# Optimization experiments

Hardware: AMD Instinct MI355X
Metric: run time of the kernel (lower is better)

The kernel has to match this reference:

```python
import jax, jax.numpy as jnp
import numpy as np

B, S, D = 4, 2048, 512
QKD = 256
HID = 3 * D  # expansion_factor=3
EPS = 1e-5


def _ln(x, g, b):
    m = jnp.mean(x, axis=-1, keepdims=True)
    v = jnp.mean((x - m) ** 2, axis=-1, keepdims=True)
    return (x - m) * jax.lax.rsqrt(v + EPS) * g + b


def setup_inputs() -> dict:
    key = jax.random.key(0)
    ks = jax.random.split(key, 12)
    s = lambda fan: 1.0 / np.sqrt(fan)
    return {
        "x":  jax.random.normal(ks[0], (B, S, D), jnp.float32),
        "Wm": jax.random.uniform(ks[1], (D, D), jnp.float32, -s(D), s(D)),
        "bm": jnp.zeros((D,), jnp.float32),
        "g1": jnp.ones((D,), jnp.float32),
        "b1": jnp.zeros((D,), jnp.float32),
        "Wh": jax.random.uniform(ks[2], (2 * HID, D), jnp.float32, -s(D), s(D)),
        "bh": jnp.zeros((2 * HID,), jnp.float32),
        "Wq": jax.random.uniform(ks[3], (QKD, D), jnp.float32, -s(D), s(D)),
        "bq": jnp.zeros((QKD,), jnp.float32),
        "Wb": jax.random.normal(ks[4], (QKD, QKD), jnp.float32),
        "Wo": jax.random.uniform(ks[5], (D, HID), jnp.float32, -s(HID), s(HID)),
        "bo": jnp.zeros((D,), jnp.float32),
        "g2": jnp.ones((D,), jnp.float32),
        "b2": jnp.zeros((D,), jnp.float32),
    }


def reference(x, Wm, bm, g1, b1, Wh, bh, Wq, bq, Wb, Wo, bo, g2, b2):
    seq_len = x.shape[-2]
    memory = jnp.einsum('bsd,ed->bse', x, Wm) + bm
    normed = _ln(x + memory, g1, b1)
    h = jax.nn.relu(jnp.einsum('bsd,hd->bsh', normed, Wh) + bh)
    v, gate = h[..., :HID], h[..., HID:]
    Z = jax.nn.relu(jnp.einsum('bsd,qd->bsq', normed, Wq) + bq)  # [B,S,QKD]
    QK = jnp.einsum('bid,de,bje->bij', Z, Wb, Z) / seq_len
    A = jax.nn.relu(QK) ** 2  # relu^2 attention, no softmax
    V = jnp.einsum('bij,bjd->bid', A, v) * gate
    out = _ln(jnp.einsum('bsh,dh->bsd', V, Wo) + bo, g2, b2)
    return out + x
```

## Files before the change

kernel.cpp:

```cpp
#include <hip/hip_runtime.h>

typedef unsigned short u16;
typedef unsigned char u8;
typedef __attribute__((ext_vector_type(8))) short short8;
typedef __attribute__((ext_vector_type(4))) float f32x4;
typedef __attribute__((ext_vector_type(8))) int int8v;
typedef __attribute__((ext_vector_type(4))) int int4v;

#define LN_EPS 1e-5f
#define SCALE_A 4096.f
#define SCALE_V 8.f
#define INV_SCALE_AV (1.f/32768.f)
#define MX_ONE 0x7F7F7F7Fu

__device__ __forceinline__ u16 f2bf(float f){
    union { float f; unsigned u; } c; c.f = f;
    unsigned u = c.u + 0x7FFFu + ((c.u >> 16) & 1u);
    return (u16)(u >> 16);
}
__device__ __forceinline__ float bf2f(u16 h){
    union { unsigned u; float f; } c; c.u = ((unsigned)h) << 16;
    return c.f;
}
__device__ __forceinline__ u8 f2fp8(float f){
    int r = __builtin_amdgcn_cvt_pk_fp8_f32(f, 0.f, 0, false);
    return (u8)(r & 0xFF);
}

enum { EPI_NONE=0, EPI_BIAS_RES, EPI_RELUSQ };
enum { OT_F32=0, OT_BF16=1, OT_FP8=2 };

__device__ __forceinline__ void gl2lds16(const void* g, void* lds){
    __builtin_amdgcn_global_load_lds(
        (const __attribute__((address_space(1))) unsigned*)g,
        (__attribute__((address_space(3))) unsigned*)lds, 16, 0, 0);
}

template<int EPI, int OT>
__global__ __launch_bounds__(256)
void mgemm(const u16* __restrict__ A, const u16* __restrict__ B, void* __restrict__ Cv,
           int K, int lda, int ldb, int ldc,
           long sAb, long sBb, long sCb,
           const float* __restrict__ bias,
           const float* __restrict__ ext, int ldext,
           float scale)
{
    __shared__ u16 sA[2][4096];
    __shared__ u16 sB[2][4096];
    const int tid = threadIdx.x;
    const int m0 = blockIdx.y * 128, n0 = blockIdx.x * 128;
    const int z  = blockIdx.z;
    const u16* Az = A + (size_t)z * sAb;
    const u16* Bz = B + (size_t)z * sBb;

    const int lane = tid & 63, quad = lane >> 4, l15 = lane & 15;
    const int wave = tid >> 6;
    const int wm = (wave >> 1) * 64, wn = (wave & 1) * 64;

    const u16* gA[2]; const u16* gB[2]; int lo[2];
#pragma unroll
    for (int r = 0; r < 2; r++){
        const int c = tid + r * 256;
        gA[r] = Az + (size_t)(m0 + (c & 127)) * lda + (c >> 7) * 8;
        gB[r] = Bz + (size_t)(n0 + (c & 127)) * ldb + (c >> 7) * 8;
        lo[r] = ((tid & 192) + r * 256) * 16;
    }

    auto stage = [&](int buf, int k0){
#pragma unroll
        for (int r = 0; r < 2; r++){
            gl2lds16(gA[r] + k0, (char*)sA[buf] + lo[r]);
            gl2lds16(gB[r] + k0, (char*)sB[buf] + lo[r]);
        }
    };

    f32x4 acc[4][4];
#pragma unroll
    for (int i = 0; i < 4; i++)
#pragma unroll
        for (int j = 0; j < 4; j++) acc[i][j] = (f32x4){0.f,0.f,0.f,0.f};

    stage(0, 0);
    int buf = 0;
    for (int k0 = 0; k0 < K; k0 += 32){
        __syncthreads();
        if (k0 + 32 < K) stage(buf ^ 1, k0 + 32);
        const u16* fA = sA[buf] + quad * 1024 + (wm + l15) * 8;
        const u16* fB = sB[buf] + quad * 1024 + (wn + l15) * 8;
        short8 a[4], b[4];
#pragma unroll
        for (int t = 0; t < 4; t++){
            a[t] = *(const short8*)(fA + t * 128);
            b[t] = *(const short8*)(fB + t * 128);
        }
#pragma unroll
        for (int i = 0; i < 4; i++)
#pragma unroll
            for (int j = 0; j < 4; j++)
                acc[i][j] = __builtin_amdgcn_mfma_f32_16x16x32_bf16(a[i], b[j], acc[i][j], 0, 0, 0);
        buf ^= 1;
    }

    float* Cf = (float*)Cv; u16* Ch = (u16*)Cv; u8* C8 = (u8*)Cv;
    const size_t zc = (size_t)z * sCb;
#pragma unroll
    for (int i = 0; i < 4; i++){
#pragma unroll
        for (int j = 0; j < 4; j++){
            const int n = n0 + wn + j * 16 + l15;
            float bs = (EPI==EPI_BIAS_RES) ? bias[n] : 0.f;
#pragma unroll
            for (int r = 0; r < 4; r++){
                const int m = m0 + wm + i * 16 + quad * 4 + r;
                float v = acc[i][j][r] + bs;
                if (EPI==EPI_BIAS_RES)
                    v += ext[(size_t)m * ldext + n];
                if (EPI==EPI_RELUSQ){ float t = fmaxf(v * scale, 0.f); v = t * t * SCALE_A; }
                if (OT==OT_FP8)       C8[zc + (size_t)m * ldc + n] = f2fp8(v);
                else if (OT==OT_BF16) Ch[zc + (size_t)m * ldc + n] = f2bf(v);
                else                  Cf[zc + (size_t)m * ldc + n] = v;
            }
        }
    }
}

__global__ __launch_bounds__(256)
void mgemm_dual(const u16* __restrict__ Anrm, const u16* __restrict__ Wh,
                const u16* __restrict__ Wq,
                const float* __restrict__ bh, const float* __restrict__ bq,
                u8* __restrict__ v8, u16* __restrict__ gbf, u16* __restrict__ Zb)
{
    __shared__ u16 sA[2][4096];
    __shared__ u16 sB[2][4096];
    const int tid = threadIdx.x;
    const bool isZ = blockIdx.x >= 24;
    const u16* Bm = isZ ? Wq : Wh;
    const float* bias = isZ ? bq : bh;
    const int m0 = blockIdx.y * 128;
    const int n0 = (isZ ? (blockIdx.x - 24) : blockIdx.x) * 128;
    const int K = 512, lda = 512, ldb = 512;

    const int lane = tid & 63, quad = lane >> 4, l15 = lane & 15;
    const int wave = tid >> 6;
    const int wm = (wave >> 1) * 64, wn = (wave & 1) * 64;

    const u16* gA[2]; const u16* gB[2]; int lo[2];
#pragma unroll
    for (int r = 0; r < 2; r++){
        const int c = tid + r * 256;
        gA[r] = Anrm + (size_t)(m0 + (c & 127)) * lda + (c >> 7) * 8;
        gB[r] = Bm   + (size_t)(n0 + (c & 127)) * ldb + (c >> 7) * 8;
        lo[r] = ((tid & 192) + r * 256) * 16;
    }
    auto stage = [&](int buf, int k0){
#pragma unroll
        for (int r = 0; r < 2; r++){
            gl2lds16(gA[r] + k0, (char*)sA[buf] + lo[r]);
            gl2lds16(gB[r] + k0, (char*)sB[buf] + lo[r]);
        }
    };

    f32x4 acc[4][4];
#pragma unroll
    for (int i = 0; i < 4; i++)
#pragma unroll
        for (int j = 0; j < 4; j++) acc[i][j] = (f32x4){0.f,0.f,0.f,0.f};

    stage(0, 0);
    int buf = 0;
    for (int k0 = 0; k0 < K; k0 += 32){
        __syncthreads();
        if (k0 + 32 < K) stage(buf ^ 1, k0 + 32);
        const u16* fA = sA[buf] + quad * 1024 + (wm + l15) * 8;
        const u16* fB = sB[buf] + quad * 1024 + (wn + l15) * 8;
        short8 a[4], b[4];
#pragma unroll
        for (int t = 0; t < 4; t++){
            a[t] = *(const short8*)(fA + t * 128);
            b[t] = *(const short8*)(fB + t * 128);
        }
#pragma unroll
        for (int i = 0; i < 4; i++)
#pragma unroll
            for (int j = 0; j < 4; j++)
                acc[i][j] = __builtin_amdgcn_mfma_f32_16x16x32_bf16(a[i], b[j], acc[i][j], 0, 0, 0);
        buf ^= 1;
    }

#pragma unroll
    for (int i = 0; i < 4; i++){
#pragma unroll
        for (int j = 0; j < 4; j++){
            const int n = n0 + wn + j * 16 + l15;
            const float bs = bias[n];
#pragma unroll
            for (int r = 0; r < 4; r++){
                const int m = m0 + wm + i * 16 + quad * 4 + r;
                float v = fmaxf(acc[i][j][r] + bs, 0.f);
                if (isZ)            Zb[(size_t)m * 256 + n] = f2bf(v);
                else if (n < 1536)  v8[(size_t)m * 1536 + n] = f2fp8(v * SCALE_V);
                else                gbf[(size_t)m * 1536 + n - 1536] = f2bf(v);
            }
        }
    }
}

__global__ __launch_bounds__(256)
void mgemm8mx(const u8* __restrict__ A, const u8* __restrict__ B, u16* __restrict__ C,
              int K, int lda, int ldb, int ldc,
              long sAb, long sBb, long sCb,
              const u16* __restrict__ gate, int ldext, long sEb)
{
    __shared__ u8 sA[16384];
    __shared__ u8 sB[16384];
    const int tid = threadIdx.x;
    const int m0 = blockIdx.y * 128, n0 = blockIdx.x * 128;
    const int z  = blockIdx.z;
    const u8* Az = A + (size_t)z * sAb;
    const u8* Bz = B + (size_t)z * sBb;

    const int lane = tid & 63, quad = lane >> 4, l15 = lane & 15;
    const int wave = tid >> 6;
    const int wm = (wave >> 1) * 64, wn = (wave & 1) * 64;

    const u8* gA[4]; const u8* gB[4]; int lo[4];
#pragma unroll
    for (int p = 0; p < 4; p++){
        const int r = p * 32 + (tid >> 3);
        const int j = (tid & 7) ^ (r & 7);
        gA[p] = Az + (size_t)(m0 + r) * lda + j * 16;
        gB[p] = Bz + (size_t)(n0 + r) * ldb + j * 16;
        lo[p] = p * 4096 + wave * 1024;
    }

    f32x4 acc[4][4];
#pragma unroll
    for (int i = 0; i < 4; i++)
#pragma unroll
        for (int j = 0; j < 4; j++) acc[i][j] = (f32x4){0.f,0.f,0.f,0.f};

    for (int k0 = 0; k0 < K; k0 += 128){
#pragma unroll
        for (int p = 0; p < 4; p++){
            gl2lds16(gA[p] + k0, (char*)sA + lo[p]);
            gl2lds16(gB[p] + k0, (char*)sB + lo[p]);
        }
        __syncthreads();
        int8v a[4], b[4];
#pragma unroll
        for (int i = 0; i < 4; i++){
            const int m = wm + i * 16 + l15;
            const int4v a0 = *(const int4v*)(sA + m * 128 + ((2*quad    ) ^ (m & 7)) * 16);
            const int4v a1 = *(const int4v*)(sA + m * 128 + ((2*quad + 1) ^ (m & 7)) * 16);
            a[i] = (int8v){a0[0],a0[1],a0[2],a0[3],a1[0],a1[1],a1[2],a1[3]};
            const int n = wn + i * 16 + l15;
            const int4v b0 = *(const int4v*)(sB + n * 128 + ((2*quad    ) ^ (n & 7)) * 16);
            const int4v b1 = *(const int4v*)(sB + n * 128 + ((2*quad + 1) ^ (n & 7)) * 16);
            b[i] = (int8v){b0[0],b0[1],b0[2],b0[3],b1[0],b1[1],b1[2],b1[3]};
        }
#pragma unroll
        for (int i = 0; i < 4; i++)
#pragma unroll
            for (int j = 0; j < 4; j++)
                acc[i][j] = __builtin_amdgcn_mfma_scale_f32_16x16x128_f8f6f4(
                    a[i], b[j], acc[i][j], 0, 0, 0, MX_ONE, 0, MX_ONE);
        __syncthreads();
    }

    const size_t zc = (size_t)z * sCb;
#pragma unroll
    for (int i = 0; i < 4; i++){
#pragma unroll
        for (int j = 0; j < 4; j++){
            const int n = n0 + wn + j * 16 + l15;
#pragma unroll
            for (int r = 0; r < 4; r++){
                const int m = m0 + wm + i * 16 + quad * 4 + r;
                float v = acc[i][j][r] * INV_SCALE_AV
                        * bf2f(gate[(size_t)z * sEb + (size_t)m * ldext + n]);
                C[zc + (size_t)m * ldc + n] = f2bf(v);
            }
        }
    }
}

template<bool OUT_BF, bool POST_RES, int NSUM, bool PRE_RES>
__global__ __launch_bounds__(256)
void ln_k(const float* __restrict__ in, const float* __restrict__ g,
          const float* __restrict__ b, const float* __restrict__ res_post,
          const float* __restrict__ res_pre, const float* __restrict__ bias2,
          long pstride, void* __restrict__ out)
{
    const int row = blockIdx.x, tid = threadIdx.x;
    const size_t base = (size_t)row * 512 + tid * 2;
    float2 v = *(const float2*)(in + base);
#pragma unroll
    for (int p = 1; p < NSUM; p++){
        const float2 w = *(const float2*)(in + (size_t)p * pstride + base);
        v.x += w.x; v.y += w.y;
    }
    if (NSUM > 1){
        const float2 bb2 = *(const float2*)(bias2 + tid * 2);
        v.x += bb2.x; v.y += bb2.y;
    }
    if (PRE_RES){
        const float2 r = *(const float2*)(res_pre + base);
        v.x += r.x; v.y += r.y;
    }
    float s = v.x + v.y, ss = v.x * v.x + v.y * v.y;
#pragma unroll
    for (int off = 32; off > 0; off >>= 1){
        s  += __shfl_down(s,  off);
        ss += __shfl_down(ss, off);
    }
    __shared__ float sbuf[8], ssbuf[8];
    const int wid = tid >> 6, lane = tid & 63;
    if (lane == 0){ sbuf[wid] = s; ssbuf[wid] = ss; }
    __syncthreads();
    if (tid == 0){
        float S = 0.f, SS = 0.f;
#pragma unroll
        for (int i = 0; i < 4; i++){ S += sbuf[i]; SS += ssbuf[i]; }
        const float mean = S * (1.f/512.f);
        const float var  = SS * (1.f/512.f) - mean * mean;
        sbuf[4]  = mean;
        ssbuf[4] = rsqrtf(var + LN_EPS);
    }
    __syncthreads();
    const float mean = sbuf[4], rstd = ssbuf[4];
    const float2 gg = *(const float2*)(g + tid * 2);
    const float2 bb = *(const float2*)(b + tid * 2);
    float ox = (v.x - mean) * rstd * gg.x + bb.x;
    float oy = (v.y - mean) * rstd * gg.y + bb.y;
    if (POST_RES){
        const float2 r = *(const float2*)(res_post + base);
        ox += r.x; oy += r.y;
    }
    if (OUT_BF){
        unsigned pk = ((unsigned)f2bf(oy) << 16) | (unsigned)f2bf(ox);
        ((unsigned*)out)[(size_t)row * 256 + tid] = pk;
    } else {
        *(float2*)((float*)out + base) = make_float2(ox, oy);
    }
}

__global__ __launch_bounds__(256)
void castall_k(const float* __restrict__ x, const float* __restrict__ Wm,
               const float* __restrict__ Wh, const float* __restrict__ Wq,
               const float* __restrict__ Wo, const float* __restrict__ Wb,
               u16* __restrict__ xb, u16* __restrict__ Wmb, u16* __restrict__ Whb,
               u16* __restrict__ Wqb, u16* __restrict__ Wob, u16* __restrict__ WbT)
{
    const int i = blockIdx.x * 256 + threadIdx.x;
    if (i >= 1736704){
        const int j = i - 1736704;
        if (j < 65536){
            const int e = j >> 8, d = j & 255;
            WbT[e * 256 + d] = f2bf(Wb[d * 256 + e]);
        }
        return;
    }
    const float* src; u16* dst; int off;
    if      (i < 1048576){ src = x;  dst = xb;  off = i; }
    else if (i < 1114112){ src = Wm; dst = Wmb; off = i - 1048576; }
    else if (i < 1507328){ src = Wh; dst = Whb; off = i - 1114112; }
    else if (i < 1540096){ src = Wq; dst = Wqb; off = i - 1507328; }
    else                 { src = Wo; dst = Wob; off = i - 1540096; }
    const float4 v = ((const float4*)src)[off];
    ushort4 o; o.x = f2bf(v.x); o.y = f2bf(v.y); o.z = f2bf(v.z); o.w = f2bf(v.w);
    ((ushort4*)dst)[off] = o;
}

__global__ __launch_bounds__(256)
void tr8_k(const u8* __restrict__ v, u8* __restrict__ vT, int S, int HID){
    const int b = blockIdx.z;
    const int h0 = blockIdx.x * 64, s0 = blockIdx.y * 64;
    __shared__ u8 t[64][68];
    const u8* vb = v + (size_t)b * S * HID;
    u8* vTb = vT + (size_t)b * HID * S;
    const int tid = threadIdx.x;
#pragma unroll
    for (int i = 0; i < 4; i++){
        int idx = tid + i * 256;
        int r = idx >> 4, c4 = (idx & 15) * 4;
        uchar4 u = *(const uchar4*)(vb + (size_t)(s0 + r) * HID + h0 + c4);
        t[r][c4] = u.x; t[r][c4+1] = u.y; t[r][c4+2] = u.z; t[r][c4+3] = u.w;
    }
    __syncthreads();
#pragma unroll
    for (int i = 0; i < 4; i++){
        int idx = tid + i * 256;
        int r = idx >> 4, c4 = (idx & 15) * 4;
        uchar4 u;
        u.x = t[c4][r]; u.y = t[c4+1][r]; u.z = t[c4+2][r]; u.w = t[c4+3][r];
        *(uchar4*)(vTb + (size_t)(h0 + r) * S + s0 + c4) = u;
    }
}

extern "C" void kernel_launch(void* const* d_in, const int* in_sizes, int n_in,
                              void* d_out, int out_size, void* d_ws, size_t ws_size,
                              hipStream_t stream)
{
    const float* x  = (const float*)d_in[0];
    const float* Wm = (const float*)d_in[1];
    const float* bm = (const float*)d_in[2];
    const float* g1 = (const float*)d_in[3];
    const float* b1 = (const float*)d_in[4];
    const float* Wh = (const float*)d_in[5];
    const float* bh = (const float*)d_in[6];
    const float* Wq = (const float*)d_in[7];
    const float* bq = (const float*)d_in[8];
    const float* Wb = (const float*)d_in[9];
    const float* Wo = (const float*)d_in[10];
    const float* bo = (const float*)d_in[11];
    const float* g2 = (const float*)d_in[12];
    const float* b2 = (const float*)d_in[13];
    float* out = (float*)d_out;
    (void)in_sizes; (void)n_in; (void)out_size; (void)ws_size;

    const int Bn=4, S=2048, D=512, QKD=256, HID=1536, H2=3072;
    const int M = Bn * S;
    const long MD = (long)M * D;

    char* p = (char*)d_ws;
    auto alloc = [&](size_t bytes)->void*{ void* r = p; p += (bytes + 255) & ~(size_t)255; return r; };
    u16*  xbf  = (u16*) alloc((size_t)M*D*2);
    u16*  Wmbf = (u16*) alloc((size_t)D*D*2);
    u16*  Whbf = (u16*) alloc((size_t)H2*D*2);
    u16*  Wqbf = (u16*) alloc((size_t)QKD*D*2);
    u16*  Wobf = (u16*) alloc((size_t)D*HID*2);
    u16*  WbT  = (u16*) alloc((size_t)QKD*QKD*2);
    float* ybuf= (float*)alloc((size_t)MD*4*3);
    u16*  Zb   = (u16*) alloc((size_t)M*QKD*2);
    u16*  ZWbb = (u16*) alloc((size_t)M*QKD*2);
    u8*   v8   = (u8*)  alloc((size_t)M*HID);
    u16*  gbf  = (u16*) alloc((size_t)M*HID*2);
    u8*   vT8  = (u8*)  alloc((size_t)M*HID);
    u8*   A8   = (u8*)  alloc((size_t)M*S);
    u16*  Vgbf = (u16*) alloc((size_t)M*HID*2);
    u16*  nrm  = xbf;

    dim3 blk(256);

    castall_k<<<dim3(7040), blk, 0, stream>>>(x, Wm, Wh, Wq, Wo, Wb,
                                              xbf, Wmbf, Whbf, Wqbf, Wobf, WbT);
    mgemm<EPI_BIAS_RES,OT_F32><<<dim3(D/128, M/128, 1), blk, 0, stream>>>(
        xbf, Wmbf, ybuf, D, D, D, D, 0,0,0, bm, x, D, 1.f);
    ln_k<true,false,1,false><<<dim3(M), blk, 0, stream>>>(
        ybuf, g1, b1, nullptr, nullptr, nullptr, 0, nrm);
    mgemm_dual<<<dim3(26, M/128), blk, 0, stream>>>(
        nrm, Whbf, Wqbf, bh, bq, v8, gbf, Zb);
    mgemm<EPI_NONE,OT_BF16><<<dim3(QKD/128, M/128, 1), blk, 0, stream>>>(
        Zb, WbT, ZWbb, QKD, QKD, QKD, QKD, 0,0,0, nullptr, nullptr, 0, 1.f);
    mgemm<EPI_RELUSQ,OT_FP8><<<dim3(S/128, S/128, Bn), blk, 0, stream>>>(
        ZWbb, Zb, A8, QKD, QKD, QKD, S,
        (long)S*QKD, (long)S*QKD, (long)S*S,
        nullptr, nullptr, 0, 1.f/(float)S);
    tr8_k<<<dim3(HID/64, S/64, Bn), blk, 0, stream>>>(v8, vT8, S, HID);
    mgemm8mx<<<dim3(HID/128, S/128, Bn), blk, 0, stream>>>(
        A8, vT8, Vgbf, S, S, S, HID,
        (long)S*S, (long)HID*S, (long)S*HID,
        gbf, HID, (long)S*HID);
    mgemm<EPI_NONE,OT_F32><<<dim3(D/128, M/128, 3), blk, 0, stream>>>(
        Vgbf, Wobf, ybuf, HID/3, HID, HID, D, 512, 512, MD,
        nullptr, nullptr, 0, 1.f);
    ln_k<false,true,3,false><<<dim3(M), blk, 0, stream>>>(
        ybuf, g2, b2, x, nullptr, bo, MD, out);
}
```

Baseline: 341.7 us.

## Compute value projection in MX fp8 and rework GEMM staging and output split-K

The value half of the Wh projection now runs through the fp8 MX GEMM, fed by a new fp8 copy of the normed activations and fp8 Wh weights. Only the gate half and Wq stay in the bf16 dual GEMM. The bf16 GEMMs drop LDS double buffering in favour of a single buffer with two barriers per k-step, which lowers LDS use and may raise occupancy but removes load/compute overlap. The Wo projection changes from 3-way to 2-way split-K with bf16 partials, and the final layernorm is specialised, cutting intermediate memory traffic at some precision cost.

```diff
diff --git a/kernel.cpp b/kernel.cpp
--- a/kernel.cpp
+++ b/kernel.cpp
@@ -11,6 +11,9 @@
 #define SCALE_A 4096.f
 #define SCALE_V 8.f
 #define INV_SCALE_AV (1.f/32768.f)
+#define SCALE_NRM 4.f
+#define SCALE_WH 512.f
+#define INV_SCALE_H (1.f/2048.f)
 #define MX_ONE 0x7F7F7F7Fu
 
 __device__ __forceinline__ u16 f2bf(float f){
@@ -26,8 +29,12 @@
     int r = __builtin_amdgcn_cvt_pk_fp8_f32(f, 0.f, 0, false);
     return (u8)(r & 0xFF);
 }
-
-enum { EPI_NONE=0, EPI_BIAS_RES, EPI_RELUSQ };
+__device__ __forceinline__ u16 f2fp8x2(float a, float b){
+    int r = __builtin_amdgcn_cvt_pk_fp8_f32(a, b, 0, false);
+    return (u16)(r & 0xFFFF);
+}
+
+enum { EPI_NONE=0, EPI_BIAS_RES, EPI_BIAS_RELU, EPI_RELUSQ };
 enum { OT_F32=0, OT_BF16=1, OT_FP8=2 };
 
 __device__ __forceinline__ void gl2lds16(const void* g, void* lds){
@@ -45,8 +52,8 @@
            const float* __restrict__ ext, int ldext,
            float scale)
 {
-    __shared__ u16 sA[2][4096];
-    __shared__ u16 sB[2][4096];
+    __shared__ u16 sA[4096];
+    __shared__ u16 sB[4096];
     const int tid = threadIdx.x;
     const int m0 = blockIdx.y * 128, n0 = blockIdx.x * 128;
     const int z  = blockIdx.z;
@@ -66,27 +73,22 @@
         lo[r] = ((tid & 192) + r * 256) * 16;
     }
 
-    auto stage = [&](int buf, int k0){
+    f32x4 acc[4][4];
+#pragma unroll
+    for (int i = 0; i < 4; i++)
+#pragma unroll
+        for (int j = 0; j < 4; j++) acc[i][j] = (f32x4){0.f,0.f,0.f,0.f};
+
+    const u16* fA = sA + quad * 1024 + (wm + l15) * 8;
+    const u16* fB = sB + quad * 1024 + (wn + l15) * 8;
+
+    for (int k0 = 0; k0 < K; k0 += 32){
 #pragma unroll
         for (int r = 0; r < 2; r++){
-            gl2lds16(gA[r] + k0, (char*)sA[buf] + lo[r]);
-            gl2lds16(gB[r] + k0, (char*)sB[buf] + lo[r]);
-        }
-    };
-
-    f32x4 acc[4][4];
-#pragma unroll
-    for (int i = 0; i < 4; i++)
-#pragma unroll
-        for (int j = 0; j < 4; j++) acc[i][j] = (f32x4){0.f,0.f,0.f,0.f};
-
-    stage(0, 0);
-    int buf = 0;
-    for (int k0 = 0; k0 < K; k0 += 32){
+            gl2lds16(gA[r] + k0, (char*)sA + lo[r]);
+            gl2lds16(gB[r] + k0, (char*)sB + lo[r]);
+        }
         __syncthreads();
-        if (k0 + 32 < K) stage(buf ^ 1, k0 + 32);
-        const u16* fA = sA[buf] + quad * 1024 + (wm + l15) * 8;
-        const u16* fB = sB[buf] + quad * 1024 + (wn + l15) * 8;
         short8 a[4], b[4];
 #pragma unroll
         for (int t = 0; t < 4; t++){
@@ -98,7 +100,7 @@
 #pragma unroll
             for (int j = 0; j < 4; j++)
                 acc[i][j] = __builtin_amdgcn_mfma_f32_16x16x32_bf16(a[i], b[j], acc[i][j], 0, 0, 0);
-        buf ^= 1;
+        __syncthreads();
     }
 
     float* Cf = (float*)Cv; u16* Ch = (u16*)Cv; u8* C8 = (u8*)Cv;
@@ -108,13 +110,15 @@
 #pragma unroll
         for (int j = 0; j < 4; j++){
             const int n = n0 + wn + j * 16 + l15;
-            float bs = (EPI==EPI_BIAS_RES) ? bias[n] : 0.f;
+            float bs = (EPI==EPI_BIAS_RES || EPI==EPI_BIAS_RELU) ? bias[n] : 0.f;
 #pragma unroll
             for (int r = 0; r < 4; r++){
                 const int m = m0 + wm + i * 16 + quad * 4 + r;
                 float v = acc[i][j][r] + bs;
                 if (EPI==EPI_BIAS_RES)
                     v += ext[(size_t)m * ldext + n];
+                if (EPI==EPI_BIAS_RELU)
+                    v = fmaxf(v, 0.f);
                 if (EPI==EPI_RELUSQ){ float t = fmaxf(v * scale, 0.f); v = t * t * SCALE_A; }
                 if (OT==OT_FP8)       C8[zc + (size_t)m * ldc + n] = f2fp8(v);
                 else if (OT==OT_BF16) Ch[zc + (size_t)m * ldc + n] = f2bf(v);
@@ -125,19 +129,19 @@
 }
 
 __global__ __launch_bounds__(256)
-void mgemm_dual(const u16* __restrict__ Anrm, const u16* __restrict__ Wh,
+void mgemm_dual(const u16* __restrict__ Anrm, const u16* __restrict__ Whg,
                 const u16* __restrict__ Wq,
-                const float* __restrict__ bh, const float* __restrict__ bq,
-                u8* __restrict__ v8, u16* __restrict__ gbf, u16* __restrict__ Zb)
-{
-    __shared__ u16 sA[2][4096];
-    __shared__ u16 sB[2][4096];
+                const float* __restrict__ bhg, const float* __restrict__ bq,
+                u16* __restrict__ gbf, u16* __restrict__ Zb)
+{
+    __shared__ u16 sA[4096];
+    __shared__ u16 sB[4096];
     const int tid = threadIdx.x;
-    const bool isZ = blockIdx.x >= 24;
-    const u16* Bm = isZ ? Wq : Wh;
-    const float* bias = isZ ? bq : bh;
+    const bool isZ = blockIdx.x >= 12;
+    const u16* Bm = isZ ? Wq : Whg;
+    const float* bias = isZ ? bq : bhg;
     const int m0 = blockIdx.y * 128;
-    const int n0 = (isZ ? (blockIdx.x - 24) : blockIdx.x) * 128;
+    const int n0 = (isZ ? (blockIdx.x - 12) : blockIdx.x) * 128;
     const int K = 512, lda = 512, ldb = 512;
 
     const int lane = tid & 63, quad = lane >> 4, l15 = lane & 15;
@@ -152,27 +156,23 @@
         gB[r] = Bm   + (size_t)(n0 + (c & 127)) * ldb + (c >> 7) * 8;
         lo[r] = ((tid & 192) + r * 256) * 16;
     }
-    auto stage = [&](int buf, int k0){
+
+    f32x4 acc[4][4];
+#pragma unroll
+    for (int i = 0; i < 4; i++)
+#pragma unroll
+        for (int j = 0; j < 4; j++) acc[i][j] = (f32x4){0.f,0.f,0.f,0.f};
+
+    const u16* fA = sA + quad * 1024 + (wm + l15) * 8;
+    const u16* fB = sB + quad * 1024 + (wn + l15) * 8;
+
+    for (int k0 = 0; k0 < K; k0 += 32){
 #pragma unroll
         for (int r = 0; r < 2; r++){
-            gl2lds16(gA[r] + k0, (char*)sA[buf] + lo[r]);
-            gl2lds16(gB[r] + k0, (char*)sB[buf] + lo[r]);
-        }
-    };
-
-    f32x4 acc[4][4];
-#pragma unroll
-    for (int i = 0; i < 4; i++)
-#pragma unroll
-        for (int j = 0; j < 4; j++) acc[i][j] = (f32x4){0.f,0.f,0.f,0.f};
-
-    stage(0, 0);
-    int buf = 0;
-    for (int k0 = 0; k0 < K; k0 += 32){
+            gl2lds16(gA[r] + k0, (char*)sA + lo[r]);
+            gl2lds16(gB[r] + k0, (char*)sB + lo[r]);
+        }
         __syncthreads();
-        if (k0 + 32 < K) stage(buf ^ 1, k0 + 32);
-        const u16* fA = sA[buf] + quad * 1024 + (wm + l15) * 8;
-        const u16* fB = sB[buf] + quad * 1024 + (wn + l15) * 8;
         short8 a[4], b[4];
 #pragma unroll
         for (int t = 0; t < 4; t++){
@@ -184,7 +184,7 @@
 #pragma unroll
             for (int j = 0; j < 4; j++)
                 acc[i][j] = __builtin_amdgcn_mfma_f32_16x16x32_bf16(a[i], b[j], acc[i][j], 0, 0, 0);
-        buf ^= 1;
+        __syncthreads();
     }
 
 #pragma unroll
@@ -197,19 +197,20 @@
             for (int r = 0; r < 4; r++){
                 const int m = m0 + wm + i * 16 + quad * 4 + r;
                 float v = fmaxf(acc[i][j][r] + bs, 0.f);
-                if (isZ)            Zb[(size_t)m * 256 + n] = f2bf(v);
-                else if (n < 1536)  v8[(size_t)m * 1536 + n] = f2fp8(v * SCALE_V);
-                else                gbf[(size_t)m * 1536 + n - 1536] = f2bf(v);
+                if (isZ) Zb[(size_t)m * 256 + n] = f2bf(v);
+                else     gbf[(size_t)m * 1536 + n] = f2bf(v);
             }
         }
     }
 }
 
+template<bool VOUT>
 __global__ __launch_bounds__(256)
 void mgemm8mx(const u8* __restrict__ A, const u8* __restrict__ B, u16* __restrict__ C,
               int K, int lda, int ldb, int ldc,
               long sAb, long sBb, long sCb,
-              const u16* __restrict__ gate, int ldext, long sEb)
+              const u16* __restrict__ gate, int ldext, long sEb,
+              const float* __restrict__ bias, u8* __restrict__ vout)
 {
     __shared__ u8 sA[16384];
     __shared__ u8 sB[16384];
@@ -276,37 +277,26 @@
 #pragma unroll
             for (int r = 0; r < 4; r++){
                 const int m = m0 + wm + i * 16 + quad * 4 + r;
-                float v = acc[i][j][r] * INV_SCALE_AV
-                        * bf2f(gate[(size_t)z * sEb + (size_t)m * ldext + n]);
-                C[zc + (size_t)m * ldc + n] = f2bf(v);
+                if (VOUT){
+                    float h = fmaxf(acc[i][j][r] * INV_SCALE_H + bias[n], 0.f);
+                    vout[(size_t)m * 1536 + n] = f2fp8(h * SCALE_V);
+                } else {
+                    float v = acc[i][j][r] * INV_SCALE_AV
+                            * bf2f(gate[(size_t)z * sEb + (size_t)m * ldext + n]);
+                    C[zc + (size_t)m * ldc + n] = f2bf(v);
+                }
             }
         }
     }
 }
 
-template<bool OUT_BF, bool POST_RES, int NSUM, bool PRE_RES>
-__global__ __launch_bounds__(256)
-void ln_k(const float* __restrict__ in, const float* __restrict__ g,
-          const float* __restrict__ b, const float* __restrict__ res_post,
-          const float* __restrict__ res_pre, const float* __restrict__ bias2,
-          long pstride, void* __restrict__ out)
+__global__ __launch_bounds__(256)
+void ln1_k(const float* __restrict__ in, const float* __restrict__ g,
+           const float* __restrict__ b, u16* __restrict__ nbf, u16* __restrict__ n8)
 {
     const int row = blockIdx.x, tid = threadIdx.x;
     const size_t base = (size_t)row * 512 + tid * 2;
-    float2 v = *(const float2*)(in + base);
-#pragma unroll
-    for (int p = 1; p < NSUM; p++){
-        const float2 w = *(const float2*)(in + (size_t)p * pstride + base);
-        v.x += w.x; v.y += w.y;
-    }
-    if (NSUM > 1){
-        const float2 bb2 = *(const float2*)(bias2 + tid * 2);
-        v.x += bb2.x; v.y += bb2.y;
-    }
-    if (PRE_RES){
-        const float2 r = *(const float2*)(res_pre + base);
-        v.x += r.x; v.y += r.y;
-    }
+    const float2 v = *(const float2*)(in + base);
     float s = v.x + v.y, ss = v.x * v.x + v.y * v.y;
 #pragma unroll
     for (int off = 32; off > 0; off >>= 1){
@@ -330,25 +320,63 @@
     const float mean = sbuf[4], rstd = ssbuf[4];
     const float2 gg = *(const float2*)(g + tid * 2);
     const float2 bb = *(const float2*)(b + tid * 2);
-    float ox = (v.x - mean) * rstd * gg.x + bb.x;
-    float oy = (v.y - mean) * rstd * gg.y + bb.y;
-    if (POST_RES){
-        const float2 r = *(const float2*)(res_post + base);
-        ox += r.x; oy += r.y;
-    }
-    if (OUT_BF){
-        unsigned pk = ((unsigned)f2bf(oy) << 16) | (unsigned)f2bf(ox);
-        ((unsigned*)out)[(size_t)row * 256 + tid] = pk;
-    } else {
-        *(float2*)((float*)out + base) = make_float2(ox, oy);
-    }
+    const float ox = (v.x - mean) * rstd * gg.x + bb.x;
+    const float oy = (v.y - mean) * rstd * gg.y + bb.y;
+    ((unsigned*)nbf)[(size_t)row * 256 + tid] =
+        ((unsigned)f2bf(oy) << 16) | (unsigned)f2bf(ox);
+    n8[(size_t)row * 256 + tid] = f2fp8x2(ox * SCALE_NRM, oy * SCALE_NRM);
+}
+
+__global__ __launch_bounds__(256)
+void ln2_k(const u16* __restrict__ pa, long pstride,
+           const float* __restrict__ bias2,
+           const float* __restrict__ g, const float* __restrict__ b,
+           const float* __restrict__ x, float* __restrict__ out)
+{
+    const int row = blockIdx.x, tid = threadIdx.x;
+    const size_t base = (size_t)row * 512 + tid * 2;
+    const unsigned p0 = ((const unsigned*)pa)[(size_t)row * 256 + tid];
+    const unsigned p1 = ((const unsigned*)(pa + pstride))[(size_t)row * 256 + tid];
+    const float2 bb2 = *(const float2*)(bias2 + tid * 2);
+    float2 v;
+    v.x = bf2f((u16)p0) + bf2f((u16)p1) + bb2.x;
+    v.y = bf2f((u16)(p0 >> 16)) + bf2f((u16)(p1 >> 16)) + bb2.y;
+    float s = v.x + v.y, ss = v.x * v.x + v.y * v.y;
+#pragma unroll
+    for (int off = 32; off > 0; off >>= 1){
+        s  += __shfl_down(s,  off);
+        ss += __shfl_down(ss, off);
+    }
+    __shared__ float sbuf[8], ssbuf[8];
+    const int wid = tid >> 6, lane = tid & 63;
+    if (lane == 0){ sbuf[wid] = s; ssbuf[wid] = ss; }
+    __syncthreads();
+    if (tid == 0){
+        float S = 0.f, SS = 0.f;
+#pragma unroll
+        for (int i = 0; i < 4; i++){ S += sbuf[i]; SS += ssbuf[i]; }
+        const float mean = S * (1.f/512.f);
+        const float var  = SS * (1.f/512.f) - mean * mean;
+        sbuf[4]  = mean;
+        ssbuf[4] = rsqrtf(var + LN_EPS);
+    }
+    __syncthreads();
+    const float mean = sbuf[4], rstd = ssbuf[4];
+    const float2 gg = *(const float2*)(g + tid * 2);
+    const float2 bb = *(const float2*)(b + tid * 2);
+    const float2 r = *(const float2*)(x + base);
+    float2 o;
+    o.x = (v.x - mean) * rstd * gg.x + bb.x + r.x;
+    o.y = (v.y - mean) * rstd * gg.y + bb.y + r.y;
+    *(float2*)(out + base) = o;
 }
 
 __global__ __launch_bounds__(256)
 void castall_k(const float* __restrict__ x, const float* __restrict__ Wm,
                const float* __restrict__ Wh, const float* __restrict__ Wq,
                const float* __restrict__ Wo, const float* __restrict__ Wb,
-               u16* __restrict__ xb, u16* __restrict__ Wmb, u16* __restrict__ Whb,
+               u16* __restrict__ xb, u16* __restrict__ Wmb, u8* __restrict__ Wh8,
+               u16* __restrict__ Whgb,
                u16* __restrict__ Wqb, u16* __restrict__ Wob, u16* __restrict__ WbT)
 {
     const int i = blockIdx.x * 256 + threadIdx.x;
@@ -360,12 +388,20 @@
         }
         return;
     }
+    if (i >= 1114112 && i < 1310720){
+        const int off = i - 1114112;
+        const float4 v = ((const float4*)Wh)[off];
+        unsigned r0 = (unsigned)f2fp8x2(v.x * SCALE_WH, v.y * SCALE_WH);
+        unsigned r1 = (unsigned)f2fp8x2(v.z * SCALE_WH, v.w * SCALE_WH);
+        ((unsigned*)Wh8)[off] = r0 | (r1 << 16);
+        return;
+    }
     const float* src; u16* dst; int off;
-    if      (i < 1048576){ src = x;  dst = xb;  off = i; }
-    else if (i < 1114112){ src = Wm; dst = Wmb; off = i - 1048576; }
-    else if (i < 1507328){ src = Wh; dst = Whb; off = i - 1114112; }
-    else if (i < 1540096){ src = Wq; dst = Wqb; off = i - 1507328; }
-    else                 { src = Wo; dst = Wob; off = i - 1540096; }
+    if      (i < 1048576){ src = x;  dst = xb;   off = i; }
+    else if (i < 1114112){ src = Wm; dst = Wmb;  off = i - 1048576; }
+    else if (i < 1507328){ src = Wh + 786432; dst = Whgb; off = i - 1310720; }
+    else if (i < 1540096){ src = Wq; dst = Wqb;  off = i - 1507328; }
+    else                 { src = Wo; dst = Wob;  off = i - 1540096; }
     const float4 v = ((const float4*)src)[off];
     ushort4 o; o.x = f2bf(v.x); o.y = f2bf(v.y); o.z = f2bf(v.z); o.w = f2bf(v.w);
     ((ushort4*)dst)[off] = o;
@@ -418,7 +454,7 @@
     float* out = (float*)d_out;
     (void)in_sizes; (void)n_in; (void)out_size; (void)ws_size;
 
-    const int Bn=4, S=2048, D=512, QKD=256, HID=1536, H2=3072;
+    const int Bn=4, S=2048, D=512, QKD=256, HID=1536;
     const int M = Bn * S;
     const long MD = (long)M * D;
 
@@ -426,11 +462,14 @@
     auto alloc = [&](size_t bytes)->void*{ void* r = p; p += (bytes + 255) & ~(size_t)255; return r; };
     u16*  xbf  = (u16*) alloc((size_t)M*D*2);
     u16*  Wmbf = (u16*) alloc((size_t)D*D*2);
-    u16*  Whbf = (u16*) alloc((size_t)H2*D*2);
+    u8*   Wh8  = (u8*)  alloc((size_t)HID*D);
+    u16*  Whgb = (u16*) alloc((size_t)HID*D*2);
     u16*  Wqbf = (u16*) alloc((size_t)QKD*D*2);
     u16*  Wobf = (u16*) alloc((size_t)D*HID*2);
     u16*  WbT  = (u16*) alloc((size_t)QKD*QKD*2);
-    float* ybuf= (float*)alloc((size_t)MD*4*3);
+    float* ybuf= (float*)alloc((size_t)MD*4);
+    u16*  wop  = (u16*) alloc((size_t)MD*2*2);
+    u16*  n8   = (u16*) alloc((size_t)M*D);
     u16*  Zb   = (u16*) alloc((size_t)M*QKD*2);
     u16*  ZWbb = (u16*) alloc((size_t)M*QKD*2);
     u8*   v8   = (u8*)  alloc((size_t)M*HID);
@@ -443,13 +482,15 @@
     dim3 blk(256);
 
     castall_k<<<dim3(7040), blk, 0, stream>>>(x, Wm, Wh, Wq, Wo, Wb,
-                                              xbf, Wmbf, Whbf, Wqbf, Wobf, WbT);
+                                              xbf, Wmbf, Wh8, Whgb, Wqbf, Wobf, WbT);
     mgemm<EPI_BIAS_RES,OT_F32><<<dim3(D/128, M/128, 1), blk, 0, stream>>>(
         xbf, Wmbf, ybuf, D, D, D, D, 0,0,0, bm, x, D, 1.f);
-    ln_k<true,false,1,false><<<dim3(M), blk, 0, stream>>>(
-        ybuf, g1, b1, nullptr, nullptr, nullptr, 0, nrm);
-    mgemm_dual<<<dim3(26, M/128), blk, 0, stream>>>(
-        nrm, Whbf, Wqbf, bh, bq, v8, gbf, Zb);
+    ln1_k<<<dim3(M), blk, 0, stream>>>(ybuf, g1, b1, nrm, n8);
+    mgemm8mx<true><<<dim3(HID/128, M/128, 1), blk, 0, stream>>>(
+        (const u8*)n8, Wh8, nullptr, D, D, D, 0, 0,0,0,
+        nullptr, 0, 0, bh, v8);
+    mgemm_dual<<<dim3(14, M/128), blk, 0, stream>>>(
+        nrm, Whgb, Wqbf, bh + HID, bq, gbf, Zb);
     mgemm<EPI_NONE,OT_BF16><<<dim3(QKD/128, M/128, 1), blk, 0, stream>>>(
         Zb, WbT, ZWbb, QKD, QKD, QKD, QKD, 0,0,0, nullptr, nullptr, 0, 1.f);
     mgemm<EPI_RELUSQ,OT_FP8><<<dim3(S/128, S/128, Bn), blk, 0, stream>>>(
@@ -457,13 +498,12 @@
         (long)S*QKD, (long)S*QKD, (long)S*S,
         nullptr, nullptr, 0, 1.f/(float)S);
     tr8_k<<<dim3(HID/64, S/64, Bn), blk, 0, stream>>>(v8, vT8, S, HID);
-    mgemm8mx<<<dim3(HID/128, S/128, Bn), blk, 0, stream>>>(
+    mgemm8mx<false><<<dim3(HID/128, S/128, Bn), blk, 0, stream>>>(
         A8, vT8, Vgbf, S, S, S, HID,
         (long)S*S, (long)HID*S, (long)S*HID,
-        gbf, HID, (long)S*HID);
-    mgemm<EPI_NONE,OT_F32><<<dim3(D/128, M/128, 3), blk, 0, stream>>>(
-        Vgbf, Wobf, ybuf, HID/3, HID, HID, D, 512, 512, MD,
+        gbf, HID, (long)S*HID, nullptr, nullptr);
+    mgemm<EPI_NONE,OT_BF16><<<dim3(D/128, M/128, 2), blk, 0, stream>>>(
+        Vgbf, Wobf, wop, HID/2, HID, HID, D, 768, 768, MD,
         nullptr, nullptr, 0, 1.f);
-    ln_k<false,true,3,false><<<dim3(M), blk, 0, stream>>>(
-        ybuf, g2, b2, x, nullptr, bo, MD, out);
-}
+    ln2_k<<<dim3(M), blk, 0, stream>>>(wop, MD, bo, g2, b2, x, out);
+}
```

Measured after the change: 312.7 us. 8.5% less time.
